# Performance work log

Hardware: AMD Instinct MI355X
Metric: run time of the kernel (lower is better)

## Reference

```python
import jax, jax.numpy as jnp
import numpy as np
from jax import lax

MD = 4  # correlation max displacement -> (2*MD+1)**2 = 81 channels
BACKWARP_COEF = 1.25  # level 4 entry in the coefficient table


def leaky(x):
    return jnp.where(x >= 0, x, 0.1 * x)


def conv3x3(x, w, b):
    # x: [B,Cin,H,W], w: [Cout,Cin,3,3]
    y = lax.conv_general_dilated(x, w, (1, 1), [(1, 1), (1, 1)],
                                 dimension_numbers=('NCHW', 'OIHW', 'NCHW'))
    return y + b[None, :, None, None]


def deconv4x4_s2(x, w, b):
    # torch ConvTranspose2d(k=4, s=2, p=1); w: [Cin,Cout,4,4]
    y = lax.conv_general_dilated(x, w[:, :, ::-1, ::-1], (1, 1), [(2, 2), (2, 2)],
                                 lhs_dilation=(2, 2),
                                 dimension_numbers=('NCHW', 'IOHW', 'NCHW'))
    return y + b[None, :, None, None]


def grid_sample_zeros(img, grid):
    # bilinear, padding_mode='zeros', align_corners=False
    B, C, H, W = img.shape
    x = (grid[..., 0] + 1.0) * 0.5 * W - 0.5  # [B,H,W]
    y = (grid[..., 1] + 1.0) * 0.5 * H - 0.5
    x0 = jnp.floor(x); y0 = jnp.floor(y)
    wx1 = x - x0; wx0 = 1.0 - wx1
    wy1 = y - y0; wy0 = 1.0 - wy1

    def gather(ix, iy):
        valid = (ix >= 0) & (ix < W) & (iy >= 0) & (iy < H)
        ixc = jnp.clip(ix, 0, W - 1).astype(jnp.int32)
        iyc = jnp.clip(iy, 0, H - 1).astype(jnp.int32)
        v = jax.vmap(lambda im, yy, xx: im[:, yy, xx])(img, iyc, ixc)  # [B,C,H,W]
        return jnp.where(valid[:, None], v, 0.0)

    out = (gather(x0, y0) * (wx0 * wy0)[:, None]
           + gather(x0 + 1, y0) * (wx1 * wy0)[:, None]
           + gather(x0, y0 + 1) * (wx0 * wy1)[:, None]
           + gather(x0 + 1, y0 + 1) * (wx1 * wy1)[:, None])
    return out


def backwarp(feat, flow):
    B, C, H, W = feat.shape
    gx = jnp.linspace(-1.0 + 1.0 / W, 1.0 - 1.0 / W, W, dtype=feat.dtype)
    gy = jnp.linspace(-1.0 + 1.0 / H, 1.0 - 1.0 / H, H, dtype=feat.dtype)
    fx = flow[:, 0] / ((W - 1.0) / 2.0)
    fy = flow[:, 1] / ((H - 1.0) / 2.0)
    grid = jnp.stack([gx[None, None, :] + fx, gy[None, :, None] + fy], axis=-1)  # [B,H,W,2]
    feat1 = jnp.concatenate([feat, jnp.ones((B, 1, H, W), feat.dtype)], axis=1)
    out = grid_sample_zeros(feat1, grid)
    mask = jnp.where(out[:, -1:] > 0.999, 1.0, 0.0).astype(feat.dtype)
    return out[:, :-1] * mask


def correlation(f1, f2):
    # PWC-Net cost volume: mean over channels of shifted products, 81 shifts
    B, C, H, W = f1.shape
    f2p = jnp.pad(f2, ((0, 0), (0, 0), (MD, MD), (MD, MD)))
    outs = []
    for dy in range(2 * MD + 1):
        for dx in range(2 * MD + 1):
            outs.append(jnp.mean(f1 * f2p[:, :, dy:dy + H, dx:dx + W], axis=1))
    return jnp.stack(outs, axis=1)  # [B,81,H,W]


def setup_inputs() -> dict:
    key = jax.random.key(0)
    ks = jax.random.split(key, 24)
    B, C, H, W = 16, 48, 64, 128
    cc = 81 + 48 + 2 + 2  # 133
    prev_feat_c = 81 + 48 + 48 + 24 + 16  # 217
    p = lambda k, s: jax.random.normal(k, s, dtype=jnp.float32) * 0.05
    return {
        'feat_1': jax.random.normal(ks[0], (B, C, H, W), dtype=jnp.float32),
        'feat_2': jax.random.normal(ks[1], (B, C, H, W), dtype=jnp.float32),
        'prev_flow': jax.random.normal(ks[2], (B, 2, H // 2, W // 2), dtype=jnp.float32),
        'prev_feat': jax.random.normal(ks[3], (B, prev_feat_c, H // 2, W // 2), dtype=jnp.float32),
        'w1': p(ks[4], (48, cc, 3, 3)), 'b1': p(ks[5], (48,)),
        'w2': p(ks[6], (48, cc + 48, 3, 3)), 'b2': p(ks[7], (48,)),
        'w3': p(ks[8], (24, cc + 96, 3, 3)), 'b3': p(ks[9], (24,)),
        'w4': p(ks[10], (16, cc + 120, 3, 3)), 'b4': p(ks[11], (16,)),
        'w5': p(ks[12], (2, cc + 136, 3, 3)), 'b5': p(ks[13], (2,)),
        'w_upflow': p(ks[14], (2, 2, 4, 4)), 'b_upflow': p(ks[15], (2,)),
        'w_upfeat': p(ks[16], (prev_feat_c, 2, 4, 4)), 'b_upfeat': p(ks[17], (2,)),
    }


def reference(feat_1, feat_2, prev_flow, prev_feat,
              w1, b1, w2, b2, w3, b3, w4, b4, w5, b5,
              w_upflow, b_upflow, w_upfeat, b_upfeat):
    upped_flow = deconv4x4_s2(prev_flow, w_upflow, b_upflow)   # [B,2,H,W]
    upped_feat = deconv4x4_s2(prev_feat, w_upfeat, b_upfeat)   # [B,2,H,W]
    warped_feat_2 = backwarp(feat_2, upped_flow * BACKWARP_COEF)
    corr_volume = leaky(correlation(feat_1, warped_feat_2))    # [B,81,H,W]
    feat_out = jnp.concatenate([corr_volume, feat_1, upped_flow, upped_feat], axis=1)
    feat_out = jnp.concatenate([leaky(conv3x3(feat_out, w1, b1)), feat_out], axis=1)
    feat_out = jnp.concatenate([leaky(conv3x3(feat_out, w2, b2)), feat_out], axis=1)
    feat_out = jnp.concatenate([leaky(conv3x3(feat_out, w3, b3)), feat_out], axis=1)
    feat_out = jnp.concatenate([leaky(conv3x3(feat_out, w4, b4)), feat_out], axis=1)
    flow = leaky(conv3x3(feat_out, w5, b5))
    return flow, feat_out
```

## Files before the change

kernel.cpp:

```cpp
#include <hip/hip_runtime.h>


#define DEVFN __device__ __forceinline__

constexpr int B = 16, H = 64, W = 128, HW = H * W;
constexpr int CF = 48;
constexpr int PFC = 217;
constexpr int H2 = 32, W2 = 64, HW2 = H2 * W2;
constexpr int FC = 269;
constexpr int FCP = 272;
constexpr int FLOW_ELEMS = B * 2 * HW;

constexpr int OFF_CORR = 136, OFF_F1 = 217, OFF_UF = 265, OFF_UPFEAT = 267;
constexpr int FB_F1 = 136, FB_CORR = 184;

constexpr size_t WS_ZEROS = 0;
constexpr size_t WS_FEATB = 256;
constexpr size_t FEATB_BYTES = (size_t)B * HW * FCP * 2;
constexpr size_t WS_WARPEDH = WS_FEATB + FEATB_BYTES;
constexpr size_t WARPEDH_BYTES = (size_t)3 * B * HW * 16 * 2;
constexpr size_t WS_PART = WS_WARPEDH + WARPEDH_BYTES;
constexpr size_t PART_BYTES = (size_t)7 * B * 2 * HW * 4;
constexpr size_t WS_WB = WS_PART + PART_BYTES;

typedef short bf16x8 __attribute__((ext_vector_type(8)));
typedef float f32x4 __attribute__((ext_vector_type(4)));
typedef _Float16 h16x2 __attribute__((ext_vector_type(2)));
typedef _Float16 h16x8 __attribute__((ext_vector_type(8)));

DEVFN float leaky(float x) { return x >= 0.f ? x : 0.1f * x; }

DEVFN unsigned short f2b(float f) {
  unsigned int u = __float_as_uint(f);
  u += 0x7FFFu + ((u >> 16) & 1u);
  return (unsigned short)(u >> 16);
}

DEVFN void gload16(const void* g, void* l) {
  __builtin_amdgcn_global_load_lds(
      (const __attribute__((address_space(1))) void*)g,
      (__attribute__((address_space(3))) void*)l, 16, 0, 0);
}

DEVFN int featb2ref(int p) {
  if (p >= FB_F1 && p < FB_CORR) return OFF_F1 + (p - FB_F1);
  if (p >= FB_CORR && p < 265) return OFF_CORR + (p - FB_CORR);
  return p;
}

__global__ __launch_bounds__(256) void k_repack_all(
    const float* __restrict__ w1, const float* __restrict__ w2,
    const float* __restrict__ w3, const float* __restrict__ w4,
    const float* __restrict__ w5,
    unsigned short* __restrict__ wb1, unsigned short* __restrict__ wb2,
    unsigned short* __restrict__ wb3, unsigned short* __restrict__ wb4,
    unsigned short* __restrict__ wb5, unsigned short* __restrict__ zeros) {
  int blk = blockIdx.x;
  if (blk == 0 && threadIdx.x < 32) zeros[threadIdx.x] = 0;
  const float* w;
  unsigned short* wb;
  int CIN, COUT, COUTP, IN_OFF, rbase;
  if (blk < 270)       { w = w1; wb = wb1; CIN = 133; COUT = 48; COUTP = 48; IN_OFF = 136; rbase = 0; }
  else if (blk < 594)  { w = w2; wb = wb2; CIN = 181; COUT = 48; COUTP = 48; IN_OFF = 88;  rbase = 270; }
  else if (blk < 882)  { w = w3; wb = wb3; CIN = 229; COUT = 24; COUTP = 32; IN_OFF = 40;  rbase = 594; }
  else if (blk < 1026) { w = w4; wb = wb4; CIN = 253; COUT = 16; COUTP = 16; IN_OFF = 16;  rbase = 882; }
  else                 { w = w5; wb = wb5; CIN = 269; COUT = 2;  COUTP = 16; IN_OFF = 0;   rbase = 1026; }
  int e = (blk - rbase) * 256 + threadIdx.x;
  int nchunk = (CIN + 31) >> 5;
  int TOT = nchunk * 9 * COUTP * 32;
  if (e >= TOT) return;
  int j = e & 7, qpos = (e >> 3) & 3;
  int row = e >> 5;
  int co = row % COUTP;
  int tapch = row / COUTP;
  int tap = tapch % 9, ch = tapch / 9;
  int k = ch * 32 + ((qpos ^ ((co >> 1) & 3)) << 3) + j;
  float v = 0.f;
  if (co < COUT && k < CIN) {
    int ci = featb2ref(IN_OFF + k) - IN_OFF;
    v = w[(co * CIN + ci) * 9 + tap];
  }
  wb[e] = f2b(v);
}

__global__ __launch_bounds__(256) void k_dcf_dflow(
    const float* __restrict__ pfeat, const float* __restrict__ wup,
    const float* __restrict__ pflow, const float* __restrict__ wuf,
    const float* __restrict__ buf_, float* __restrict__ partial,
    float* __restrict__ feat, unsigned short* __restrict__ featb) {
  __shared__ float wl[1024];
  __shared__ float red[2048];
  int tid = threadIdx.x;
  if (blockIdx.x >= 3584) {
    int t = (blockIdx.x - 3584) * 256 + tid;
    if (t >= B * 2 * HW) return;
    int x = t % W, y = (t / W) % H, co = (t / HW) % 2, b = t / (2 * HW);
    float acc = buf_[co];
    int ky0 = ((y & 1) == 0) ? 1 : 0;
    int kx0 = ((x & 1) == 0) ? 1 : 0;
#pragma unroll
    for (int kyi = 0; kyi < 2; ++kyi) {
      int ky = ky0 + 2 * kyi;
      int iy = (y + 1 - ky) >> 1;
      if (iy < 0 || iy >= H2) continue;
#pragma unroll
      for (int kxi = 0; kxi < 2; ++kxi) {
        int kx = kx0 + 2 * kxi;
        int ix = (x + 1 - kx) >> 1;
        if (ix < 0 || ix >= W2) continue;
#pragma unroll
        for (int ci = 0; ci < 2; ++ci)
          acc += pflow[(b * 2 + ci) * HW2 + iy * W2 + ix] *
                 wuf[((ci * 2 + co) * 4 + ky) * 4 + kx];
      }
    }
    int pix = (b * H + y) * W + x;
    feat[(b * FC + OFF_UF + co) * HW + y * W + x] = acc;
    featb[pix * FCP + OFF_UF + co] = f2b(acc);
    if (co == 0) {
      featb[pix * FCP + 269] = 0;
      featb[pix * FCP + 270] = 0;
      featb[pix * FCP + 271] = 0;
    }
    return;
  }
  int blk = blockIdx.x;
  int chunk = blk % 7, t2 = blk / 7;
  int y2 = t2 % H2, b = t2 / H2;
  int ch0 = chunk * 32;
  for (int i = tid; i < 1024; i += 256) {
    int ci = ch0 + (i >> 5);
    wl[i] = (ci < PFC) ? wup[ci * 32 + (i & 31)] : 0.f;
  }
  __syncthreads();
  int x2 = tid & 63, cg = tid >> 6;
  float acc[8];
#pragma unroll
  for (int v = 0; v < 8; ++v) acc[v] = 0.f;
#pragma unroll 1
  for (int k = 0; k < 8; ++k) {
    int cil = cg * 8 + k;
    int ci = ch0 + cil;
    bool cv = ci < PFC;
    const float* src = pfeat + ((size_t)b * PFC + ci) * HW2;
    float iv[3][3];
#pragma unroll
    for (int dy = -1; dy <= 1; ++dy)
#pragma unroll
      for (int dx = -1; dx <= 1; ++dx) {
        int iy = y2 + dy, ix = x2 + dx;
        float v = 0.f;
        if (cv && iy >= 0 && iy < H2 && ix >= 0 && ix < W2) v = src[iy * W2 + ix];
        iv[dy + 1][dx + 1] = v;
      }
    const float* wc = &wl[cil * 32];
#pragma unroll
    for (int co = 0; co < 2; ++co)
#pragma unroll
      for (int ry = 0; ry < 2; ++ry)
#pragma unroll
        for (int rx = 0; rx < 2; ++rx) {
          float s = acc[co * 4 + ry * 2 + rx];
#pragma unroll
          for (int dy = ry - 1; dy <= ry; ++dy) {
            int ky = 1 + ry - 2 * dy;
#pragma unroll
            for (int dx = rx - 1; dx <= rx; ++dx) {
              int kx = 1 + rx - 2 * dx;
              s += iv[dy + 1][dx + 1] * wc[co * 16 + ky * 4 + kx];
            }
          }
          acc[co * 4 + ry * 2 + rx] = s;
        }
  }
#pragma unroll
  for (int v = 0; v < 8; ++v) red[(cg * 64 + x2) * 8 + v] = acc[v];
  __syncthreads();
  for (int idx = tid; idx < 512; idx += 256) {
    int x2b = idx & 63, vi = idx >> 6;
    float s = red[(0 + x2b) * 8 + vi] + red[(64 + x2b) * 8 + vi] +
              red[(128 + x2b) * 8 + vi] + red[(192 + x2b) * 8 + vi];
    int co = vi >> 2, ry = (vi >> 1) & 1, rx = vi & 1;
    partial[(size_t)chunk * (B * 2 * HW) + (size_t)(b * 2 + co) * HW +
            (2 * y2 + ry) * W + (2 * x2b + rx)] = s;
  }
}

__global__ __launch_bounds__(256) void k_fin_backwarp(
    const float* __restrict__ partial, const float* __restrict__ bup,
    const float* __restrict__ feat2, float* __restrict__ feat,
    unsigned short* __restrict__ featb, unsigned short* __restrict__ warpedh) {
  int tid = threadIdx.x;
  if (blockIdx.x < 1024) {
    int t = blockIdx.x * 256 + tid;
    float s = 0.f;
#pragma unroll
    for (int c = 0; c < 7; ++c) s += partial[(size_t)c * (B * 2 * HW) + t];
    int rem = t % HW;
    int co = (t / HW) & 1;
    int b = t / (2 * HW);
    s += bup[co];
    feat[((size_t)b * FC + OFF_UPFEAT + co) * HW + rem] = s;
    featb[((size_t)(b * H) * W + rem) * FCP + OFF_UPFEAT + co] = f2b(s);
    return;
  }
  int t = (blockIdx.x - 1024) * 256 + tid;
  if (t >= B * HW) return;
  int x = t % W, y = (t / W) % H, b = t / HW;
  const float SX = 1.25f * (float)W / (float)(W - 1);
  const float SY = 1.25f * (float)H / (float)(H - 1);
  float fx = feat[(b * FC + OFF_UF + 0) * HW + y * W + x];
  float fy = feat[(b * FC + OFF_UF + 1) * HW + y * W + x];
  float px = (float)x + fx * SX;
  float py = (float)y + fy * SY;
  float x0f = floorf(px), y0f = floorf(py);
  int ix0 = (int)x0f, iy0 = (int)y0f;
  float wx1 = px - x0f, wx0 = 1.f - wx1;
  float wy1 = py - y0f, wy0 = 1.f - wy1;
  bool vx0 = (ix0 >= 0) & (ix0 < W), vx1 = (ix0 + 1 >= 0) & (ix0 + 1 < W);
  bool vy0 = (iy0 >= 0) & (iy0 < H), vy1 = (iy0 + 1 >= 0) & (iy0 + 1 < H);
  float w00 = (vx0 && vy0) ? wx0 * wy0 : 0.f;
  float w01 = (vx1 && vy0) ? wx1 * wy0 : 0.f;
  float w10 = (vx0 && vy1) ? wx0 * wy1 : 0.f;
  float w11 = (vx1 && vy1) ? wx1 * wy1 : 0.f;
  float wsum = w00 + w01 + w10 + w11;
  float m = wsum > 0.999f ? 1.f : 0.f;
  w00 *= m; w01 *= m; w10 *= m; w11 *= m;
  int cx0 = min(max(ix0, 0), W - 1), cx1 = min(max(ix0 + 1, 0), W - 1);
  int cy0 = min(max(iy0, 0), H - 1), cy1 = min(max(iy0 + 1, 0), H - 1);
  const float* s = feat2 + b * CF * HW;
  int o00 = cy0 * W + cx0, o01 = cy0 * W + cx1, o10 = cy1 * W + cx0, o11 = cy1 * W + cx1;
#pragma unroll 1
  for (int chunk = 0; chunk < 3; ++chunk) {
    h16x8 out0, out1;
#pragma unroll
    for (int k = 0; k < 16; ++k) {
      const float* sc = s + (chunk * 16 + k) * HW;
      float v = w00 * sc[o00] + w01 * sc[o01] + w10 * sc[o10] + w11 * sc[o11];
      if (k < 8) out0[k & 7] = (_Float16)v;
      else       out1[k & 7] = (_Float16)v;
    }
    h16x8* dst = (h16x8*)(warpedh + ((size_t)chunk * B * HW + t) * 16);
    dst[0] = out0;
    dst[1] = out1;
  }
}

__global__ __launch_bounds__(256) void k_corr(const float* __restrict__ f1,
                                              const unsigned short* __restrict__ warpedh,
                                              const unsigned short* __restrict__ zeros,
                                              float* __restrict__ feat,
                                              unsigned short* __restrict__ featb) {
  __shared__ __align__(16) unsigned short lds[5 * 136 * 16];
  const int swz = ((blockIdx.x & 7) << 7) | (blockIdx.x >> 3);
  const int y = swz & 63, b = swz >> 6;
  const int tid = threadIdx.x;
  const int px = tid >> 1, h = tid & 1;
  const int lane = tid & 63, wv = tid >> 6;
  const int pix = (b * H + y) * W + px;
  const h16x8* hp = (const h16x8*)lds;
  char* ldsc = (char*)lds;
  const float inv = 1.f / 48.f;

#pragma unroll 1
  for (int half = 0; half < 2; ++half) {
    const int R = half ? 4 : 5;
    const int dybase = half ? 5 : 0;
    const int ND = R * 9;
    float acc[45];
#pragma unroll
    for (int d = 0; d < 45; ++d) acc[d] = 0.f;
#pragma unroll 1
    for (int chunk = 0; chunk < 3; ++chunk) {
      __syncthreads();
      const int NQ = R * 136 * 2;
      for (int q0 = 0; q0 < NQ; q0 += 256) {
        int q = q0 + tid;
        if (q < NQ) {
          int pr = q >> 1, u = q & 1;
          int r = pr / 136, p = pr - r * 136;
          int sw = (p >> 2) & 1;
          int yy = y + dybase + r - 4, xx = p - 4;
          const unsigned short* src = zeros;
          if (yy >= 0 && yy < H && xx >= 0 && xx < W)
            src = warpedh + (((size_t)chunk * B * H + b * H + yy) * W + xx) * 16 +
                  (u ^ sw) * 8;
          gload16(src, ldsc + (size_t)q0 * 16 + wv * 1024 + lane * 16);
        }
      }
      float av[8];
      const int c0 = chunk * 16 + h * 8;
#pragma unroll
      for (int j = 0; j < 8; ++j)
        av[j] = f1[((size_t)b * CF + c0 + j) * HW + y * W + px];
      h16x2 fh[4];
#pragma unroll
      for (int j = 0; j < 4; ++j) {
        fh[j][0] = (_Float16)av[2 * j];
        fh[j][1] = (_Float16)av[2 * j + 1];
      }
      asm volatile("s_waitcnt vmcnt(0)" ::: "memory");
      __syncthreads();
      if (half == 0) {
#pragma unroll
        for (int j = 0; j < 8; ++j)
          feat[((size_t)b * FC + OFF_F1 + c0 + j) * HW + y * W + px] = av[j];
        uint4 qv;
        qv.x = (unsigned)f2b(av[0]) | ((unsigned)f2b(av[1]) << 16);
        qv.y = (unsigned)f2b(av[2]) | ((unsigned)f2b(av[3]) << 16);
        qv.z = (unsigned)f2b(av[4]) | ((unsigned)f2b(av[5]) << 16);
        qv.w = (unsigned)f2b(av[6]) | ((unsigned)f2b(av[7]) << 16);
        *(uint4*)(featb + (size_t)pix * FCP + FB_F1 + c0) = qv;
      }
#pragma unroll
      for (int dy = 0; dy < 5; ++dy) {
        if (dy < R) {
#pragma unroll
          for (int dx = 0; dx < 9; ++dx) {
            int p = px + dx;
            int sw = (p >> 2) & 1;
            h16x8 v = hp[((dy * 136 + p) << 1) | (h ^ sw)];
            float a = acc[dy * 9 + dx];
            a = __builtin_amdgcn_fdot2((h16x2){v[0], v[1]}, fh[0], a, false);
            a = __builtin_amdgcn_fdot2((h16x2){v[2], v[3]}, fh[1], a, false);
            a = __builtin_amdgcn_fdot2((h16x2){v[4], v[5]}, fh[2], a, false);
            a = __builtin_amdgcn_fdot2((h16x2){v[6], v[7]}, fh[3], a, false);
            acc[dy * 9 + dx] = a;
          }
        }
      }
    }
#pragma unroll
    for (int d = 0; d < 45; ++d) {
      if (d < ND) {
        float s = acc[d] + __shfl_xor(acc[d], 1);
        acc[d] = leaky(s * inv);
      }
    }
    if (h == 0) {
#pragma unroll
      for (int d = 0; d < 45; ++d)
        if (d < ND)
          feat[((size_t)b * FC + OFF_CORR + dybase * 9 + d) * HW + y * W + px] = acc[d];
    } else {
      unsigned short* fb = featb + (size_t)pix * FCP + FB_CORR + dybase * 9;
      if (half == 0) {
#pragma unroll
        for (int g = 0; g < 5; ++g) {
          uint4 qv;
          qv.x = (unsigned)f2b(acc[8 * g + 0]) | ((unsigned)f2b(acc[8 * g + 1]) << 16);
          qv.y = (unsigned)f2b(acc[8 * g + 2]) | ((unsigned)f2b(acc[8 * g + 3]) << 16);
          qv.z = (unsigned)f2b(acc[8 * g + 4]) | ((unsigned)f2b(acc[8 * g + 5]) << 16);
          qv.w = (unsigned)f2b(acc[8 * g + 6]) | ((unsigned)f2b(acc[8 * g + 7]) << 16);
          *(uint4*)(fb + 8 * g) = qv;
        }
#pragma unroll
        for (int d = 40; d < 45; ++d) fb[d] = f2b(acc[d]);
      } else {
        fb[0] = f2b(acc[0]);
        fb[1] = f2b(acc[1]);
        fb[2] = f2b(acc[2]);
#pragma unroll
        for (int g = 0; g < 4; ++g) {
          uint4 qv;
          qv.x = (unsigned)f2b(acc[3 + 8 * g + 0]) | ((unsigned)f2b(acc[3 + 8 * g + 1]) << 16);
          qv.y = (unsigned)f2b(acc[3 + 8 * g + 2]) | ((unsigned)f2b(acc[3 + 8 * g + 3]) << 16);
          qv.z = (unsigned)f2b(acc[3 + 8 * g + 4]) | ((unsigned)f2b(acc[3 + 8 * g + 5]) << 16);
          qv.w = (unsigned)f2b(acc[3 + 8 * g + 6]) | ((unsigned)f2b(acc[3 + 8 * g + 7]) << 16);
          *(uint4*)(fb + 3 + 8 * g) = qv;
        }
        fb[35] = f2b(acc[35]);
      }
    }
  }
}

template <int CIN, int NCHUNK, int COUT, int COUTP, int IN_OFF, int OUT_OFF, bool TO_FLOW>
__global__ __launch_bounds__(256) void k_conv_mfma(
    const unsigned short* __restrict__ featb, const unsigned short* __restrict__ wb,
    const float* __restrict__ bias, const unsigned short* __restrict__ zeros,
    float* __restrict__ fout, unsigned short* __restrict__ bout) {
  constexpr int NF = COUTP / 16;
  constexpr int ROWPX = 144;
  constexpr int IN_ELE = 4 * ROWPX * 32;
  constexpr int W_SLAB = 9 * COUTP * 32;
  constexpr int NWI = (W_SLAB * 2) / 1024;
  constexpr int CLIM = 264 - IN_OFF;

  __shared__ unsigned short lds[IN_ELE + W_SLAB];

  const int swz = ((blockIdx.x & 7) << 6) | (blockIdx.x >> 3);
  const int y0 = (swz & 31) * 2, b = swz >> 5;
  const int lane = threadIdx.x & 63, wv = threadIdx.x >> 6;
  const int wr = wv >> 1, wc = wv & 1;
  const int arow = lane & 15, aslc = lane >> 4;

  const unsigned short* gp[9];
  int c8a[9];
  int lofs[9];
#pragma unroll
  for (int t = 0; t < 9; ++t) {
    int i = wv + t * 4;
    int r = i / 9, seg = i - r * 9;
    int slot = seg * 16 + (lane >> 2);
    int sub8 = ((lane & 3) ^ ((slot >> 1) & 3)) << 3;
    int yy = y0 + r - 1, xx = slot - 1;
    lofs[t] = (r * ROWPX + seg * 16) * 64;
    gp[t] = zeros; c8a[t] = 1 << 20;
    if (yy >= 0 && yy < H && xx >= 0 && xx < W) {
      gp[t] = featb + ((b * H + yy) * W + xx) * FCP + IN_OFF + sub8;
      c8a[t] = sub8;
    }
  }

  int a_off[4][3];
#pragma unroll
  for (int mi = 0; mi < 4; ++mi)
#pragma unroll
    for (int kx = 0; kx < 3; ++kx) {
      int slot = (wc * 4 + mi) * 16 + arow + kx;
      a_off[mi][kx] = slot * 32 + ((aslc ^ ((slot >> 1) & 3)) << 3);
    }
  int b_off[NF];
#pragma unroll
  for (int nf = 0; nf < NF; ++nf) {
    int co = nf * 16 + arow;
    b_off[nf] = IN_ELE + co * 32 + ((aslc ^ ((co >> 1) & 3)) << 3);
  }

  f32x4 acc[4][NF];
#pragma unroll
  for (int mi = 0; mi < 4; ++mi)
#pragma unroll
    for (int nf = 0; nf < NF; ++nf) acc[mi][nf] = (f32x4){0.f, 0.f, 0.f, 0.f};

  char* ldsc = (char*)lds;

  for (int ch = 0; ch < NCHUNK; ++ch) {
    const int ci0 = ch * 32;
    __syncthreads();
#pragma unroll
    for (int t = 0; t < 9; ++t) {
      const unsigned short* g = (c8a[t] + ci0 <= CLIM) ? gp[t] + ci0 : zeros;
      gload16(g, ldsc + lofs[t]);
    }
    for (int wi = wv; wi < NWI; wi += 4)
      gload16(wb + (size_t)ch * W_SLAB + wi * 512 + lane * 8,
              ldsc + IN_ELE * 2 + wi * 1024);
    asm volatile("s_waitcnt vmcnt(0)" ::: "memory");
    __syncthreads();
#pragma unroll
    for (int ky = 0; ky < 3; ++ky) {
#pragma unroll
      for (int kx = 0; kx < 3; ++kx) {
        bf16x8 afr[4];
#pragma unroll
        for (int mi = 0; mi < 4; ++mi)
          afr[mi] = *(const bf16x8*)(lds + a_off[mi][kx] + (wr + ky) * (ROWPX * 32));
#pragma unroll
        for (int nf = 0; nf < NF; ++nf) {
          bf16x8 bfr = *(const bf16x8*)(lds + b_off[nf] + (ky * 3 + kx) * (COUTP * 32));
#pragma unroll
          for (int mi = 0; mi < 4; ++mi)
            acc[mi][nf] = __builtin_amdgcn_mfma_f32_16x16x32_bf16(
                afr[mi], bfr, acc[mi][nf], 0, 0, 0);
        }
      }
    }
  }

  const int dcol = lane & 15;
  const int yout = y0 + wr;
#pragma unroll
  for (int nf = 0; nf < NF; ++nf) {
    int co = nf * 16 + dcol;
    if (co < COUT) {
      float bv = bias[co];
#pragma unroll
      for (int mi = 0; mi < 4; ++mi) {
#pragma unroll
        for (int r = 0; r < 4; ++r) {
          int pixel = (wc * 4 + mi) * 16 + (lane >> 4) * 4 + r;
          float v = leaky(acc[mi][nf][r] + bv);
          if constexpr (TO_FLOW) {
            fout[(b * 2 + co) * HW + yout * W + pixel] = v;
          } else {
            fout[(b * FC + OUT_OFF + co) * HW + yout * W + pixel] = v;
            bout[((b * H + yout) * W + pixel) * FCP + OUT_OFF + co] = f2b(v);
          }
        }
      }
    }
  }
}

extern "C" void kernel_launch(void* const* d_in, const int* in_sizes, int n_in,
                              void* d_out, int out_size, void* d_ws, size_t ws_size,
                              hipStream_t stream) {
  (void)in_sizes; (void)n_in; (void)out_size; (void)ws_size;
  const float* feat_1 = (const float*)d_in[0];
  const float* feat_2 = (const float*)d_in[1];
  const float* prev_flow = (const float*)d_in[2];
  const float* prev_feat = (const float*)d_in[3];
  const float* w1 = (const float*)d_in[4];
  const float* b1 = (const float*)d_in[5];
  const float* w2 = (const float*)d_in[6];
  const float* b2 = (const float*)d_in[7];
  const float* w3 = (const float*)d_in[8];
  const float* b3 = (const float*)d_in[9];
  const float* w4 = (const float*)d_in[10];
  const float* b4 = (const float*)d_in[11];
  const float* w5 = (const float*)d_in[12];
  const float* b5 = (const float*)d_in[13];
  const float* w_upflow = (const float*)d_in[14];
  const float* b_upflow = (const float*)d_in[15];
  const float* w_upfeat = (const float*)d_in[16];
  const float* b_upfeat = (const float*)d_in[17];

  float* out = (float*)d_out;
  float* feat = out + FLOW_ELEMS;

  char* ws = (char*)d_ws;
  unsigned short* zeros = (unsigned short*)(ws + WS_ZEROS);
  unsigned short* featb = (unsigned short*)(ws + WS_FEATB);
  unsigned short* warpedh = (unsigned short*)(ws + WS_WARPEDH);
  float* partial = (float*)(ws + WS_PART);
  unsigned short* wb1 = (unsigned short*)(ws + WS_WB);
  unsigned short* wb2 = wb1 + 5 * 9 * 48 * 32;
  unsigned short* wb3 = wb2 + 6 * 9 * 48 * 32;
  unsigned short* wb4 = wb3 + 8 * 9 * 32 * 32;
  unsigned short* wb5 = wb4 + 8 * 9 * 16 * 32;

  k_repack_all<<<1188, 256, 0, stream>>>(w1, w2, w3, w4, w5,
                                         wb1, wb2, wb3, wb4, wb5, zeros);
  k_dcf_dflow<<<3584 + 1024, 256, 0, stream>>>(prev_feat, w_upfeat, prev_flow,
                                               w_upflow, b_upflow, partial, feat, featb);
  k_fin_backwarp<<<1024 + 512, 256, 0, stream>>>(partial, b_upfeat, feat_2,
                                                 feat, featb, warpedh);
  k_corr<<<B * H, 256, 0, stream>>>(feat_1, warpedh, zeros, feat, featb);

  k_conv_mfma<133, 5, 48, 48, 136, 88, false><<<B * H / 2, 256, 0, stream>>>(featb, wb1, b1, zeros, feat, featb);
  k_conv_mfma<181, 6, 48, 48, 88, 40, false><<<B * H / 2, 256, 0, stream>>>(featb, wb2, b2, zeros, feat, featb);
  k_conv_mfma<229, 8, 24, 32, 40, 16, false><<<B * H / 2, 256, 0, stream>>>(featb, wb3, b3, zeros, feat, featb);
  k_conv_mfma<253, 8, 16, 16, 16, 0, false><<<B * H / 2, 256, 0, stream>>>(featb, wb4, b4, zeros, feat, featb);
  k_conv_mfma<269, 9, 2, 16, 0, 0, true><<<B * H / 2, 256, 0, stream>>>(featb, wb5, b5, zeros, out, nullptr);
}
```

Measured before the change: 247.7 us.

## Merge prep kernels, split correlation halves across blocks, retile conv to 4x64 blocks

Folds the weight-repack kernel into the deconvolution prep kernel to save one launch. Splits each correlation row into two blocks, one per displacement half, which doubles the grid and cuts per-block serial work. Retiles the MFMA convs so each 128-thread block covers 4 rows by 64 columns with two output rows per wave, improving halo reuse along y at the cost of more accumulator registers and a smaller grid.

```diff
diff --git a/kernel.cpp b/kernel.cpp
--- a/kernel.cpp
+++ b/kernel.cpp
@@ -48,51 +48,51 @@
   return p;
 }
 
-__global__ __launch_bounds__(256) void k_repack_all(
+__global__ __launch_bounds__(256) void k_prep(
     const float* __restrict__ w1, const float* __restrict__ w2,
     const float* __restrict__ w3, const float* __restrict__ w4,
     const float* __restrict__ w5,
     unsigned short* __restrict__ wb1, unsigned short* __restrict__ wb2,
     unsigned short* __restrict__ wb3, unsigned short* __restrict__ wb4,
-    unsigned short* __restrict__ wb5, unsigned short* __restrict__ zeros) {
-  int blk = blockIdx.x;
-  if (blk == 0 && threadIdx.x < 32) zeros[threadIdx.x] = 0;
-  const float* w;
-  unsigned short* wb;
-  int CIN, COUT, COUTP, IN_OFF, rbase;
-  if (blk < 270)       { w = w1; wb = wb1; CIN = 133; COUT = 48; COUTP = 48; IN_OFF = 136; rbase = 0; }
-  else if (blk < 594)  { w = w2; wb = wb2; CIN = 181; COUT = 48; COUTP = 48; IN_OFF = 88;  rbase = 270; }
-  else if (blk < 882)  { w = w3; wb = wb3; CIN = 229; COUT = 24; COUTP = 32; IN_OFF = 40;  rbase = 594; }
-  else if (blk < 1026) { w = w4; wb = wb4; CIN = 253; COUT = 16; COUTP = 16; IN_OFF = 16;  rbase = 882; }
-  else                 { w = w5; wb = wb5; CIN = 269; COUT = 2;  COUTP = 16; IN_OFF = 0;   rbase = 1026; }
-  int e = (blk - rbase) * 256 + threadIdx.x;
-  int nchunk = (CIN + 31) >> 5;
-  int TOT = nchunk * 9 * COUTP * 32;
-  if (e >= TOT) return;
-  int j = e & 7, qpos = (e >> 3) & 3;
-  int row = e >> 5;
-  int co = row % COUTP;
-  int tapch = row / COUTP;
-  int tap = tapch % 9, ch = tapch / 9;
-  int k = ch * 32 + ((qpos ^ ((co >> 1) & 3)) << 3) + j;
-  float v = 0.f;
-  if (co < COUT && k < CIN) {
-    int ci = featb2ref(IN_OFF + k) - IN_OFF;
-    v = w[(co * CIN + ci) * 9 + tap];
-  }
-  wb[e] = f2b(v);
-}
-
-__global__ __launch_bounds__(256) void k_dcf_dflow(
+    unsigned short* __restrict__ wb5, unsigned short* __restrict__ zeros,
     const float* __restrict__ pfeat, const float* __restrict__ wup,
     const float* __restrict__ pflow, const float* __restrict__ wuf,
     const float* __restrict__ buf_, float* __restrict__ partial,
     float* __restrict__ feat, unsigned short* __restrict__ featb) {
   __shared__ float wl[1024];
   __shared__ float red[2048];
-  int tid = threadIdx.x;
-  if (blockIdx.x >= 3584) {
-    int t = (blockIdx.x - 3584) * 256 + tid;
+  const int tid = threadIdx.x;
+  const int gblk = blockIdx.x;
+  if (gblk < 1188) {
+    if (gblk == 0 && tid < 32) zeros[tid] = 0;
+    const float* w;
+    unsigned short* wb;
+    int CIN, COUT, COUTP, IN_OFF, rbase;
+    if (gblk < 270)       { w = w1; wb = wb1; CIN = 133; COUT = 48; COUTP = 48; IN_OFF = 136; rbase = 0; }
+    else if (gblk < 594)  { w = w2; wb = wb2; CIN = 181; COUT = 48; COUTP = 48; IN_OFF = 88;  rbase = 270; }
+    else if (gblk < 882)  { w = w3; wb = wb3; CIN = 229; COUT = 24; COUTP = 32; IN_OFF = 40;  rbase = 594; }
+    else if (gblk < 1026) { w = w4; wb = wb4; CIN = 253; COUT = 16; COUTP = 16; IN_OFF = 16;  rbase = 882; }
+    else                  { w = w5; wb = wb5; CIN = 269; COUT = 2;  COUTP = 16; IN_OFF = 0;   rbase = 1026; }
+    int e = (gblk - rbase) * 256 + tid;
+    int nchunk = (CIN + 31) >> 5;
+    int TOT = nchunk * 9 * COUTP * 32;
+    if (e >= TOT) return;
+    int j = e & 7, qpos = (e >> 3) & 3;
+    int row = e >> 5;
+    int co = row % COUTP;
+    int tapch = row / COUTP;
+    int tap = tapch % 9, ch = tapch / 9;
+    int k = ch * 32 + ((qpos ^ ((co >> 1) & 3)) << 3) + j;
+    float v = 0.f;
+    if (co < COUT && k < CIN) {
+      int ci = featb2ref(IN_OFF + k) - IN_OFF;
+      v = w[(co * CIN + ci) * 9 + tap];
+    }
+    wb[e] = f2b(v);
+    return;
+  }
+  if (gblk >= 4772) {
+    int t = (gblk - 4772) * 256 + tid;
     if (t >= B * 2 * HW) return;
     int x = t % W, y = (t / W) % H, co = (t / HW) % 2, b = t / (2 * HW);
     float acc = buf_[co];
@@ -124,7 +124,7 @@
     }
     return;
   }
-  int blk = blockIdx.x;
+  int blk = gblk - 1188;
   int chunk = blk % 7, t2 = blk / 7;
   int y2 = t2 % H2, b = t2 / H2;
   int ch0 = chunk * 32;
@@ -252,8 +252,9 @@
                                               float* __restrict__ feat,
                                               unsigned short* __restrict__ featb) {
   __shared__ __align__(16) unsigned short lds[5 * 136 * 16];
-  const int swz = ((blockIdx.x & 7) << 7) | (blockIdx.x >> 3);
-  const int y = swz & 63, b = swz >> 6;
+  const int swz = ((blockIdx.x & 7) << 8) | (blockIdx.x >> 3);
+  const int half = swz & 1;
+  const int y = (swz >> 1) & 63, b = swz >> 7;
   const int tid = threadIdx.x;
   const int px = tid >> 1, h = tid & 1;
   const int lane = tid & 63, wv = tid >> 6;
@@ -262,150 +263,151 @@
   char* ldsc = (char*)lds;
   const float inv = 1.f / 48.f;
 
+  const int R = half ? 4 : 5;
+  const int dybase = half ? 5 : 0;
+  const int ND = R * 9;
+  float acc[45];
+#pragma unroll
+  for (int d = 0; d < 45; ++d) acc[d] = 0.f;
 #pragma unroll 1
-  for (int half = 0; half < 2; ++half) {
-    const int R = half ? 4 : 5;
-    const int dybase = half ? 5 : 0;
-    const int ND = R * 9;
-    float acc[45];
-#pragma unroll
-    for (int d = 0; d < 45; ++d) acc[d] = 0.f;
-#pragma unroll 1
-    for (int chunk = 0; chunk < 3; ++chunk) {
-      __syncthreads();
-      const int NQ = R * 136 * 2;
-      for (int q0 = 0; q0 < NQ; q0 += 256) {
-        int q = q0 + tid;
-        if (q < NQ) {
-          int pr = q >> 1, u = q & 1;
-          int r = pr / 136, p = pr - r * 136;
+  for (int chunk = 0; chunk < 3; ++chunk) {
+    __syncthreads();
+    const int NQ = R * 136 * 2;
+    for (int q0 = 0; q0 < NQ; q0 += 256) {
+      int q = q0 + tid;
+      if (q < NQ) {
+        int pr = q >> 1, u = q & 1;
+        int r = pr / 136, p = pr - r * 136;
+        int sw = (p >> 2) & 1;
+        int yy = y + dybase + r - 4, xx = p - 4;
+        const unsigned short* src = zeros;
+        if (yy >= 0 && yy < H && xx >= 0 && xx < W)
+          src = warpedh + (((size_t)chunk * B * H + b * H + yy) * W + xx) * 16 +
+                (u ^ sw) * 8;
+        gload16(src, ldsc + (size_t)q0 * 16 + wv * 1024 + lane * 16);
+      }
+    }
+    float av[8];
+    const int c0 = chunk * 16 + h * 8;
+#pragma unroll
+    for (int j = 0; j < 8; ++j)
+      av[j] = f1[((size_t)b * CF + c0 + j) * HW + y * W + px];
+    h16x2 fh[4];
+#pragma unroll
+    for (int j = 0; j < 4; ++j) {
+      fh[j][0] = (_Float16)av[2 * j];
+      fh[j][1] = (_Float16)av[2 * j + 1];
+    }
+    asm volatile("s_waitcnt vmcnt(0)" ::: "memory");
+    __syncthreads();
+    if (half == 0) {
+#pragma unroll
+      for (int j = 0; j < 8; ++j)
+        feat[((size_t)b * FC + OFF_F1 + c0 + j) * HW + y * W + px] = av[j];
+      uint4 qv;
+      qv.x = (unsigned)f2b(av[0]) | ((unsigned)f2b(av[1]) << 16);
+      qv.y = (unsigned)f2b(av[2]) | ((unsigned)f2b(av[3]) << 16);
+      qv.z = (unsigned)f2b(av[4]) | ((unsigned)f2b(av[5]) << 16);
+      qv.w = (unsigned)f2b(av[6]) | ((unsigned)f2b(av[7]) << 16);
+      *(uint4*)(featb + (size_t)pix * FCP + FB_F1 + c0) = qv;
+    }
+#pragma unroll
+    for (int dy = 0; dy < 5; ++dy) {
+      if (dy < R) {
+#pragma unroll
+        for (int dx = 0; dx < 9; ++dx) {
+          int p = px + dx;
           int sw = (p >> 2) & 1;
-          int yy = y + dybase + r - 4, xx = p - 4;
-          const unsigned short* src = zeros;
-          if (yy >= 0 && yy < H && xx >= 0 && xx < W)
-            src = warpedh + (((size_t)chunk * B * H + b * H + yy) * W + xx) * 16 +
-                  (u ^ sw) * 8;
-          gload16(src, ldsc + (size_t)q0 * 16 + wv * 1024 + lane * 16);
+          h16x8 v = hp[((dy * 136 + p) << 1) | (h ^ sw)];
+          float a = acc[dy * 9 + dx];
+          a = __builtin_amdgcn_fdot2((h16x2){v[0], v[1]}, fh[0], a, false);
+          a = __builtin_amdgcn_fdot2((h16x2){v[2], v[3]}, fh[1], a, false);
+          a = __builtin_amdgcn_fdot2((h16x2){v[4], v[5]}, fh[2], a, false);
+          a = __builtin_amdgcn_fdot2((h16x2){v[6], v[7]}, fh[3], a, false);
+          acc[dy * 9 + dx] = a;
         }
       }
-      float av[8];
-      const int c0 = chunk * 16 + h * 8;
-#pragma unroll
-      for (int j = 0; j < 8; ++j)
-        av[j] = f1[((size_t)b * CF + c0 + j) * HW + y * W + px];
-      h16x2 fh[4];
-#pragma unroll
-      for (int j = 0; j < 4; ++j) {
-        fh[j][0] = (_Float16)av[2 * j];
-        fh[j][1] = (_Float16)av[2 * j + 1];
-      }
-      asm volatile("s_waitcnt vmcnt(0)" ::: "memory");
-      __syncthreads();
-      if (half == 0) {
-#pragma unroll
-        for (int j = 0; j < 8; ++j)
-          feat[((size_t)b * FC + OFF_F1 + c0 + j) * HW + y * W + px] = av[j];
+    }
+  }
+#pragma unroll
+  for (int d = 0; d < 45; ++d) {
+    if (d < ND) {
+      float s = acc[d] + __shfl_xor(acc[d], 1);
+      acc[d] = leaky(s * inv);
+    }
+  }
+  if (h == 0) {
+#pragma unroll
+    for (int d = 0; d < 45; ++d)
+      if (d < ND)
+        feat[((size_t)b * FC + OFF_CORR + dybase * 9 + d) * HW + y * W + px] = acc[d];
+  } else {
+    unsigned short* fb = featb + (size_t)pix * FCP + FB_CORR + dybase * 9;
+    if (half == 0) {
+#pragma unroll
+      for (int g = 0; g < 5; ++g) {
         uint4 qv;
-        qv.x = (unsigned)f2b(av[0]) | ((unsigned)f2b(av[1]) << 16);
-        qv.y = (unsigned)f2b(av[2]) | ((unsigned)f2b(av[3]) << 16);
-        qv.z = (unsigned)f2b(av[4]) | ((unsigned)f2b(av[5]) << 16);
-        qv.w = (unsigned)f2b(av[6]) | ((unsigned)f2b(av[7]) << 16);
-        *(uint4*)(featb + (size_t)pix * FCP + FB_F1 + c0) = qv;
-      }
-#pragma unroll
-      for (int dy = 0; dy < 5; ++dy) {
-        if (dy < R) {
-#pragma unroll
-          for (int dx = 0; dx < 9; ++dx) {
-            int p = px + dx;
-            int sw = (p >> 2) & 1;
-            h16x8 v = hp[((dy * 136 + p) << 1) | (h ^ sw)];
-            float a = acc[dy * 9 + dx];
-            a = __builtin_amdgcn_fdot2((h16x2){v[0], v[1]}, fh[0], a, false);
-            a = __builtin_amdgcn_fdot2((h16x2){v[2], v[3]}, fh[1], a, false);
-            a = __builtin_amdgcn_fdot2((h16x2){v[4], v[5]}, fh[2], a, false);
-            a = __builtin_amdgcn_fdot2((h16x2){v[6], v[7]}, fh[3], a, false);
-            acc[dy * 9 + dx] = a;
-          }
-        }
-      }
-    }
-#pragma unroll
-    for (int d = 0; d < 45; ++d) {
-      if (d < ND) {
-        float s = acc[d] + __shfl_xor(acc[d], 1);
-        acc[d] = leaky(s * inv);
-      }
-    }
-    if (h == 0) {
-#pragma unroll
-      for (int d = 0; d < 45; ++d)
-        if (d < ND)
-          feat[((size_t)b * FC + OFF_CORR + dybase * 9 + d) * HW + y * W + px] = acc[d];
+        qv.x = (unsigned)f2b(acc[8 * g + 0]) | ((unsigned)f2b(acc[8 * g + 1]) << 16);
+        qv.y = (unsigned)f2b(acc[8 * g + 2]) | ((unsigned)f2b(acc[8 * g + 3]) << 16);
+        qv.z = (unsigned)f2b(acc[8 * g + 4]) | ((unsigned)f2b(acc[8 * g + 5]) << 16);
+        qv.w = (unsigned)f2b(acc[8 * g + 6]) | ((unsigned)f2b(acc[8 * g + 7]) << 16);
+        *(uint4*)(fb + 8 * g) = qv;
+      }
+#pragma unroll
+      for (int d = 40; d < 45; ++d) fb[d] = f2b(acc[d]);
     } else {
-      unsigned short* fb = featb + (size_t)pix * FCP + FB_CORR + dybase * 9;
-      if (half == 0) {
-#pragma unroll
-        for (int g = 0; g < 5; ++g) {
-          uint4 qv;
-          qv.x = (unsigned)f2b(acc[8 * g + 0]) | ((unsigned)f2b(acc[8 * g + 1]) << 16);
-          qv.y = (unsigned)f2b(acc[8 * g + 2]) | ((unsigned)f2b(acc[8 * g + 3]) << 16);
-          qv.z = (unsigned)f2b(acc[8 * g + 4]) | ((unsigned)f2b(acc[8 * g + 5]) << 16);
-          qv.w = (unsigned)f2b(acc[8 * g + 6]) | ((unsigned)f2b(acc[8 * g + 7]) << 16);
-          *(uint4*)(fb + 8 * g) = qv;
-        }
-#pragma unroll
-        for (int d = 40; d < 45; ++d) fb[d] = f2b(acc[d]);
-      } else {
-        fb[0] = f2b(acc[0]);
-        fb[1] = f2b(acc[1]);
-        fb[2] = f2b(acc[2]);
-#pragma unroll
-        for (int g = 0; g < 4; ++g) {
-          uint4 qv;
-          qv.x = (unsigned)f2b(acc[3 + 8 * g + 0]) | ((unsigned)f2b(acc[3 + 8 * g + 1]) << 16);
-          qv.y = (unsigned)f2b(acc[3 + 8 * g + 2]) | ((unsigned)f2b(acc[3 + 8 * g + 3]) << 16);
-          qv.z = (unsigned)f2b(acc[3 + 8 * g + 4]) | ((unsigned)f2b(acc[3 + 8 * g + 5]) << 16);
-          qv.w = (unsigned)f2b(acc[3 + 8 * g + 6]) | ((unsigned)f2b(acc[3 + 8 * g + 7]) << 16);
-          *(uint4*)(fb + 3 + 8 * g) = qv;
-        }
-        fb[35] = f2b(acc[35]);
-      }
+      fb[0] = f2b(acc[0]);
+      fb[1] = f2b(acc[1]);
+      fb[2] = f2b(acc[2]);
+#pragma unroll
+      for (int g = 0; g < 4; ++g) {
+        uint4 qv;
+        qv.x = (unsigned)f2b(acc[3 + 8 * g + 0]) | ((unsigned)f2b(acc[3 + 8 * g + 1]) << 16);
+        qv.y = (unsigned)f2b(acc[3 + 8 * g + 2]) | ((unsigned)f2b(acc[3 + 8 * g + 3]) << 16);
+        qv.z = (unsigned)f2b(acc[3 + 8 * g + 4]) | ((unsigned)f2b(acc[3 + 8 * g + 5]) << 16);
+        qv.w = (unsigned)f2b(acc[3 + 8 * g + 6]) | ((unsigned)f2b(acc[3 + 8 * g + 7]) << 16);
+        *(uint4*)(fb + 3 + 8 * g) = qv;
+      }
+      fb[35] = f2b(acc[35]);
     }
   }
 }
 
 template <int CIN, int NCHUNK, int COUT, int COUTP, int IN_OFF, int OUT_OFF, bool TO_FLOW>
-__global__ __launch_bounds__(256) void k_conv_mfma(
+__global__ __launch_bounds__(128) void k_conv_mfma(
     const unsigned short* __restrict__ featb, const unsigned short* __restrict__ wb,
     const float* __restrict__ bias, const unsigned short* __restrict__ zeros,
     float* __restrict__ fout, unsigned short* __restrict__ bout) {
   constexpr int NF = COUTP / 16;
-  constexpr int ROWPX = 144;
-  constexpr int IN_ELE = 4 * ROWPX * 32;
+  constexpr int ROWPX = 68;
+  constexpr int IN_ELE = 6 * ROWPX * 32;
   constexpr int W_SLAB = 9 * COUTP * 32;
   constexpr int NWI = (W_SLAB * 2) / 1024;
   constexpr int CLIM = 264 - IN_OFF;
+  constexpr int ROWB = ROWPX * 32;
 
   __shared__ unsigned short lds[IN_ELE + W_SLAB];
 
   const int swz = ((blockIdx.x & 7) << 6) | (blockIdx.x >> 3);
-  const int y0 = (swz & 31) * 2, b = swz >> 5;
+  const int xh = swz & 1, yt = (swz >> 1) & 15, b = swz >> 5;
+  const int y0 = yt * 4, x0 = xh * 64;
   const int lane = threadIdx.x & 63, wv = threadIdx.x >> 6;
-  const int wr = wv >> 1, wc = wv & 1;
   const int arow = lane & 15, aslc = lane >> 4;
 
-  const unsigned short* gp[9];
-  int c8a[9];
-  int lofs[9];
-#pragma unroll
-  for (int t = 0; t < 9; ++t) {
-    int i = wv + t * 4;
-    int r = i / 9, seg = i - r * 9;
-    int slot = seg * 16 + (lane >> 2);
+  const unsigned short* gp[15];
+  int c8a[15];
+  int lofs[15];
+  bool a4[15];
+#pragma unroll
+  for (int t = 0; t < 15; ++t) {
+    int i = wv + 2 * t;
+    int r = i / 5, seg = i % 5;
+    int sbase = (seg < 4) ? seg * 16 : 64;
+    int slot = sbase + (lane >> 2);
     int sub8 = ((lane & 3) ^ ((slot >> 1) & 3)) << 3;
-    int yy = y0 + r - 1, xx = slot - 1;
-    lofs[t] = (r * ROWPX + seg * 16) * 64;
+    int yy = y0 + r - 1, xx = x0 + slot - 1;
+    lofs[t] = (r * ROWPX + sbase) * 64;
+    a4[t] = (seg == 4);
     gp[t] = zeros; c8a[t] = 1 << 20;
     if (yy >= 0 && yy < H && xx >= 0 && xx < W) {
       gp[t] = featb + ((b * H + yy) * W + xx) * FCP + IN_OFF + sub8;
@@ -415,11 +417,12 @@
 
   int a_off[4][3];
 #pragma unroll
-  for (int mi = 0; mi < 4; ++mi)
+  for (int xf = 0; xf < 4; ++xf)
 #pragma unroll
     for (int kx = 0; kx < 3; ++kx) {
-      int slot = (wc * 4 + mi) * 16 + arow + kx;
-      a_off[mi][kx] = slot * 32 + ((aslc ^ ((slot >> 1) & 3)) << 3);
+      int slot = xf * 16 + arow + kx;
+      a_off[xf][kx] = (2 * wv) * ROWB + slot * 32 +
+                      ((aslc ^ ((slot >> 1) & 3)) << 3);
     }
   int b_off[NF];
 #pragma unroll
@@ -428,11 +431,13 @@
     b_off[nf] = IN_ELE + co * 32 + ((aslc ^ ((co >> 1) & 3)) << 3);
   }
 
-  f32x4 acc[4][NF];
-#pragma unroll
-  for (int mi = 0; mi < 4; ++mi)
-#pragma unroll
-    for (int nf = 0; nf < NF; ++nf) acc[mi][nf] = (f32x4){0.f, 0.f, 0.f, 0.f};
+  f32x4 acc[2][4][NF];
+#pragma unroll
+  for (int r = 0; r < 2; ++r)
+#pragma unroll
+    for (int xf = 0; xf < 4; ++xf)
+#pragma unroll
+      for (int nf = 0; nf < NF; ++nf) acc[r][xf][nf] = (f32x4){0.f, 0.f, 0.f, 0.f};
 
   char* ldsc = (char*)lds;
 
@@ -440,11 +445,13 @@
     const int ci0 = ch * 32;
     __syncthreads();
 #pragma unroll
-    for (int t = 0; t < 9; ++t) {
-      const unsigned short* g = (c8a[t] + ci0 <= CLIM) ? gp[t] + ci0 : zeros;
-      gload16(g, ldsc + lofs[t]);
-    }
-    for (int wi = wv; wi < NWI; wi += 4)
+    for (int t = 0; t < 15; ++t) {
+      if (!a4[t] || lane < 16) {
+        const unsigned short* g = (c8a[t] + ci0 <= CLIM) ? gp[t] + ci0 : zeros;
+        gload16(g, ldsc + lofs[t]);
+      }
+    }
+    for (int wi = wv; wi < NWI; wi += 2)
       gload16(wb + (size_t)ch * W_SLAB + wi * 512 + lane * 8,
               ldsc + IN_ELE * 2 + wi * 1024);
     asm volatile("s_waitcnt vmcnt(0)" ::: "memory");
@@ -453,40 +460,47 @@
     for (int ky = 0; ky < 3; ++ky) {
 #pragma unroll
       for (int kx = 0; kx < 3; ++kx) {
-        bf16x8 afr[4];
-#pragma unroll
-        for (int mi = 0; mi < 4; ++mi)
-          afr[mi] = *(const bf16x8*)(lds + a_off[mi][kx] + (wr + ky) * (ROWPX * 32));
+        bf16x8 afr[2][4];
+#pragma unroll
+        for (int r = 0; r < 2; ++r)
+#pragma unroll
+          for (int xf = 0; xf < 4; ++xf)
+            afr[r][xf] = *(const bf16x8*)(lds + a_off[xf][kx] + (r + ky) * ROWB);
 #pragma unroll
         for (int nf = 0; nf < NF; ++nf) {
           bf16x8 bfr = *(const bf16x8*)(lds + b_off[nf] + (ky * 3 + kx) * (COUTP * 32));
 #pragma unroll
-          for (int mi = 0; mi < 4; ++mi)
-            acc[mi][nf] = __builtin_amdgcn_mfma_f32_16x16x32_bf16(
-                afr[mi], bfr, acc[mi][nf], 0, 0, 0);
+          for (int r = 0; r < 2; ++r)
+#pragma unroll
+            for (int xf = 0; xf < 4; ++xf)
+              acc[r][xf][nf] = __builtin_amdgcn_mfma_f32_16x16x32_bf16(
+                  afr[r][xf], bfr, acc[r][xf][nf], 0, 0, 0);
         }
       }
     }
   }
 
   const int dcol = lane & 15;
-  const int yout = y0 + wr;
 #pragma unroll
   for (int nf = 0; nf < NF; ++nf) {
     int co = nf * 16 + dcol;
     if (co < COUT) {
       float bv = bias[co];
 #pragma unroll
-      for (int mi = 0; mi < 4; ++mi) {
-#pragma unroll
-        for (int r = 0; r < 4; ++r) {
-          int pixel = (wc * 4 + mi) * 16 + (lane >> 4) * 4 + r;
-          float v = leaky(acc[mi][nf][r] + bv);
-          if constexpr (TO_FLOW) {
-            fout[(b * 2 + co) * HW + yout * W + pixel] = v;
-          } else {
-            fout[(b * FC + OUT_OFF + co) * HW + yout * W + pixel] = v;
-            bout[((b * H + yout) * W + pixel) * FCP + OUT_OFF + co] = f2b(v);
+      for (int r = 0; r < 2; ++r) {
+        int yout = y0 + 2 * wv + r;
+#pragma unroll
+        for (int xf = 0; xf < 4; ++xf) {
+#pragma unroll
+          for (int rr = 0; rr < 4; ++rr) {
+            int px = x0 + xf * 16 + (lane >> 4) * 4 + rr;
+            float v = leaky(acc[r][xf][nf][rr] + bv);
+            if constexpr (TO_FLOW) {
+              fout[(b * 2 + co) * HW + yout * W + px] = v;
+            } else {
+              fout[(b * FC + OUT_OFF + co) * HW + yout * W + px] = v;
+              bout[((b * H + yout) * W + px) * FCP + OUT_OFF + co] = f2b(v);
+            }
           }
         }
       }
@@ -531,17 +545,16 @@
   unsigned short* wb4 = wb3 + 8 * 9 * 32 * 32;
   unsigned short* wb5 = wb4 + 8 * 9 * 16 * 32;
 
-  k_repack_all<<<1188, 256, 0, stream>>>(w1, w2, w3, w4, w5,
-                                         wb1, wb2, wb3, wb4, wb5, zeros);
-  k_dcf_dflow<<<3584 + 1024, 256, 0, stream>>>(prev_feat, w_upfeat, prev_flow,
-                                               w_upflow, b_upflow, partial, feat, featb);
+  k_prep<<<1188 + 3584 + 1024, 256, 0, stream>>>(
+      w1, w2, w3, w4, w5, wb1, wb2, wb3, wb4, wb5, zeros,
+      prev_feat, w_upfeat, prev_flow, w_upflow, b_upflow, partial, feat, featb);
   k_fin_backwarp<<<1024 + 512, 256, 0, stream>>>(partial, b_upfeat, feat_2,
                                                  feat, featb, warpedh);
-  k_corr<<<B * H, 256, 0, stream>>>(feat_1, warpedh, zeros, feat, featb);
-
-  k_conv_mfma<133, 5, 48, 48, 136, 88, false><<<B * H / 2, 256, 0, stream>>>(featb, wb1, b1, zeros, feat, featb);
-  k_conv_mfma<181, 6, 48, 48, 88, 40, false><<<B * H / 2, 256, 0, stream>>>(featb, wb2, b2, zeros, feat, featb);
-  k_conv_mfma<229, 8, 24, 32, 40, 16, false><<<B * H / 2, 256, 0, stream>>>(featb, wb3, b3, zeros, feat, featb);
-  k_conv_mfma<253, 8, 16, 16, 16, 0, false><<<B * H / 2, 256, 0, stream>>>(featb, wb4, b4, zeros, feat, featb);
-  k_conv_mfma<269, 9, 2, 16, 0, 0, true><<<B * H / 2, 256, 0, stream>>>(featb, wb5, b5, zeros, out, nullptr);
-}
+  k_corr<<<B * H * 2, 256, 0, stream>>>(feat_1, warpedh, zeros, feat, featb);
+
+  k_conv_mfma<133, 5, 48, 48, 136, 88, false><<<512, 128, 0, stream>>>(featb, wb1, b1, zeros, feat, featb);
+  k_conv_mfma<181, 6, 48, 48, 88, 40, false><<<512, 128, 0, stream>>>(featb, wb2, b2, zeros, feat, featb);
+  k_conv_mfma<229, 8, 24, 32, 40, 16, false><<<512, 128, 0, stream>>>(featb, wb3, b3, zeros, feat, featb);
+  k_conv_mfma<253, 8, 16, 16, 16, 0, false><<<512, 128, 0, stream>>>(featb, wb4, b4, zeros, feat, featb);
+  k_conv_mfma<269, 9, 2, 16, 0, 0, true><<<512, 128, 0, stream>>>(featb, wb5, b5, zeros, out, nullptr);
+}
```

After: 275.9 us. 1.11x slower.
